# Kernel optimization log

Measured on AMD Instinct MI355X. Metric: run time of the kernel, lower is better.

Reference implementation:

```python
import jax, jax.numpy as jnp
import numpy as np

V_N = 50000   # nodes
E_N = 800000  # edges
DS, DV, R = 64, 8, 3
NB = 16       # rbf bases (scalar edge dim); vector edge dim = 1
DS_MSG = 2 * DS + NB      # 144
DV_MSG = 2 * DV + 1       # 17
EPS = 1e-8


def _gvp(s, Vv, Wh, Ws, bs, Wmu, Wg, bg, relu):
    # s: [E, ds_in], Vv: [E, R, dv_in]
    Vh = jnp.einsum('erd,dh->erh', Vv, Wh)                 # [E, R, h]
    vn = jnp.sqrt(jnp.sum(Vh * Vh, axis=-2) + EPS)         # [E, h]
    s_out = jnp.concatenate([s, vn], axis=-1) @ Ws + bs    # [E, ds_out]
    Vmu = jnp.einsum('erh,ho->ero', Vh, Wmu)               # [E, R, dv_out]
    gate = jax.nn.sigmoid(s_out @ Wg + bg)                 # vector gating
    V_out = Vmu * gate[:, None, :]
    if relu:
        s_out = jax.nn.relu(s_out)
    return s_out, V_out


def _make_gvp_params(key, ds_in, dv_in, ds_out, dv_out):
    h = max(dv_in, dv_out)
    ks = jax.random.split(key, 4)
    Wh = jax.random.normal(ks[0], (dv_in, h), jnp.float32) / np.sqrt(dv_in)
    Ws = jax.random.normal(ks[1], (ds_in + h, ds_out), jnp.float32) / np.sqrt(ds_in + h)
    bs = jnp.zeros((ds_out,), jnp.float32)
    Wmu = jax.random.normal(ks[2], (h, dv_out), jnp.float32) / np.sqrt(h)
    Wg = jax.random.normal(ks[3], (ds_out, dv_out), jnp.float32) / np.sqrt(ds_out)
    bg = jnp.zeros((dv_out,), jnp.float32)
    return Wh, Ws, bs, Wmu, Wg, bg


def setup_inputs() -> dict:
    key = jax.random.key(0)
    ks = jax.random.split(key, 8)
    inp = {
        's': jax.random.normal(ks[0], (V_N, DS), jnp.float32),
        'V': jax.random.normal(ks[1], (V_N, R, DV), jnp.float32),
        's_e': jax.random.normal(ks[2], (E_N, NB), jnp.float32),
        'V_e': jax.random.normal(ks[3], (E_N, R, 1), jnp.float32),
        'edge_index': jax.random.randint(ks[4], (2, E_N), 0, V_N, jnp.int64 if jax.config.jax_enable_x64 else jnp.int32),
    }
    p1 = _make_gvp_params(ks[5], DS_MSG, DV_MSG, DS, DV)
    p2 = _make_gvp_params(ks[6], DS, DV, DS, DV)
    p3 = _make_gvp_params(ks[7], DS, DV, DS, DV)
    for i, p in enumerate([p1, p2, p3], start=1):
        for name, w in zip(['Wh', 'Ws', 'bs', 'Wmu', 'Wg', 'bg'], p):
            inp[f'{name}{i}'] = w
    return inp


def reference(s, V, s_e, V_e, edge_index,
              Wh1, Ws1, bs1, Wmu1, Wg1, bg1,
              Wh2, Ws2, bs2, Wmu2, Wg2, bg2,
              Wh3, Ws3, bs3, Wmu3, Wg3, bg3):
    src, dest = edge_index[0], edge_index[1]
    s_cat = jnp.concatenate([s[src], s[dest], s_e], axis=-1)   # [E, DS_MSG]
    V_cat = jnp.concatenate([V[src], V[dest], V_e], axis=-1)   # [E, R, DV_MSG]
    s1, V1 = _gvp(s_cat, V_cat, Wh1, Ws1, bs1, Wmu1, Wg1, bg1, relu=True)
    s2, V2 = _gvp(s1, V1, Wh2, Ws2, bs2, Wmu2, Wg2, bg2, relu=True)
    s3, V3 = _gvp(s2, V2, Wh3, Ws3, bs3, Wmu3, Wg3, bg3, relu=False)
    return s3, V3
```

## Files before the change

### kernel.cpp

```cpp
#include <hip/hip_runtime.h>
#include <cstddef>

#define EN 800000
#define VN 50000

__global__ __launch_bounds__(256) void node_pre(
    const float* __restrict__ s, const float* __restrict__ V,
    const float* __restrict__ Wh1, const float* __restrict__ Ws1,
    float* __restrict__ A, float* __restrict__ B,
    float* __restrict__ VA, float* __restrict__ VB)
{
    const int tid  = threadIdx.x;
    const int lane = tid & 63;
    const int wv   = __builtin_amdgcn_readfirstlane(tid >> 6);

    float w[128];
    #pragma unroll
    for (int k = 0; k < 128; ++k) w[k] = Ws1[k * 64 + lane];

    const int hv = (lane < 51) ? (lane / 3) : 0;
    const int rv = (lane < 51) ? (lane % 3) : 0;
    float whA[8], whB[8];
    #pragma unroll
    for (int d = 0; d < 8; ++d) {
        whA[d] = Wh1[d * 17 + hv];
        whB[d] = Wh1[(8 + d) * 17 + hv];
    }

    const int nwaves = gridDim.x * 4;
    for (int v = blockIdx.x * 4 + wv; v < VN; v += nwaves) {
        const float* sv = s + (size_t)v * 64;
        float a = 0.f, b = 0.f;
        #pragma unroll
        for (int k = 0; k < 64; ++k) {
            float sk = sv[k];
            a += sk * w[k];
            b += sk * w[64 + k];
        }
        A[(size_t)v * 64 + lane] = a;
        B[(size_t)v * 64 + lane] = b;

        const float* vrow = V + (size_t)v * 24 + rv * 8;
        float va = 0.f, vb = 0.f;
        #pragma unroll
        for (int d = 0; d < 8; ++d) {
            float x = vrow[d];
            va += x * whA[d];
            vb += x * whB[d];
        }
        if (lane < 51) {
            VA[(size_t)v * 52 + lane] = va;
            VB[(size_t)v * 52 + lane] = vb;
        }
    }
}

__global__ __launch_bounds__(256, 2) void edge_kernel(
    const float* __restrict__ s_e, const float* __restrict__ V_e,
    const int* __restrict__ eidx,
    const float* __restrict__ Wh1, const float* __restrict__ Ws1, const float* __restrict__ bs1,
    const float* __restrict__ Wmu1, const float* __restrict__ Wg1, const float* __restrict__ bg1,
    const float* __restrict__ Wh2, const float* __restrict__ Ws2, const float* __restrict__ bs2,
    const float* __restrict__ Wmu2, const float* __restrict__ Wg2, const float* __restrict__ bg2,
    const float* __restrict__ Wh3, const float* __restrict__ Ws3, const float* __restrict__ bs3,
    const float* __restrict__ Wmu3, const float* __restrict__ Wg3, const float* __restrict__ bg3,
    const float* __restrict__ A, const float* __restrict__ B,
    const float* __restrict__ VA, const float* __restrict__ VB,
    float* __restrict__ out)
{
    __shared__ float buf[4][72][64];
    const int tid  = threadIdx.x;
    const int lane = tid & 63;
    const int wv   = tid >> 6;
    float (*wbuf)[64] = buf[wv];

    const int e   = blockIdx.x * 256 + tid;
    const int src = eidx[e];
    const int dst = eidx[EN + e];

    const float ve0 = V_e[(size_t)e * 3 + 0];
    const float ve1 = V_e[(size_t)e * 3 + 1];
    const float ve2 = V_e[(size_t)e * 3 + 2];

    float vmu[24];
    #pragma unroll
    for (int o = 0; o < 24; ++o) vmu[o] = 0.f;

    const float4* qa  = (const float4*)(VA + (size_t)src * 52);
    const float4* qb  = (const float4*)(VB + (size_t)dst * 52);
    const float*  w16 = Wh1 + 16 * 17;

    #pragma unroll 1
    for (int c = 0; c < 4; ++c) {
        float4 a0 = qa[3*c], a1 = qa[3*c+1], a2 = qa[3*c+2];
        float4 b0 = qb[3*c], b1 = qb[3*c+1], b2 = qb[3*c+2];
        float av[12] = {a0.x,a0.y,a0.z,a0.w, a1.x,a1.y,a1.z,a1.w, a2.x,a2.y,a2.z,a2.w};
        float bv[12] = {b0.x,b0.y,b0.z,b0.w, b1.x,b1.y,b1.z,b1.w, b2.x,b2.y,b2.z,b2.w};
        #pragma unroll
        for (int i = 0; i < 4; ++i) {
            const int h = 4*c + i;
            float ww = w16[h];
            float v0 = av[3*i+0] + bv[3*i+0] + ve0 * ww;
            float v1 = av[3*i+1] + bv[3*i+1] + ve1 * ww;
            float v2 = av[3*i+2] + bv[3*i+2] + ve2 * ww;
            wbuf[h][lane] = sqrtf(v0*v0 + v1*v1 + v2*v2 + 1e-8f);
            const float* wm = Wmu1 + h * 8;
            #pragma unroll
            for (int o = 0; o < 8; ++o) {
                float m = wm[o];
                vmu[o] += v0 * m; vmu[8+o] += v1 * m; vmu[16+o] += v2 * m;
            }
        }
    }
    {
        float4 a = qa[12], b = qb[12];
        float ww = w16[16];
        float v0 = a.x + b.x + ve0 * ww;
        float v1 = a.y + b.y + ve1 * ww;
        float v2 = a.z + b.z + ve2 * ww;
        wbuf[16][lane] = sqrtf(v0*v0 + v1*v1 + v2*v2 + 1e-8f);
        const float* wm = Wmu1 + 16 * 8;
        #pragma unroll
        for (int o = 0; o < 8; ++o) {
            float m = wm[o];
            vmu[o] += v0 * m; vmu[8+o] += v1 * m; vmu[16+o] += v2 * m;
        }
    }

    float acc[64];
    {
        const float4* fa = (const float4*)(A + (size_t)src * 64);
        const float4* fb = (const float4*)(B + (size_t)dst * 64);
        #pragma unroll
        for (int q = 0; q < 16; ++q) {
            float4 ta = fa[q], tb = fb[q];
            acc[4*q+0] = ta.x + tb.x + bs1[4*q+0];
            acc[4*q+1] = ta.y + tb.y + bs1[4*q+1];
            acc[4*q+2] = ta.z + tb.z + bs1[4*q+2];
            acc[4*q+3] = ta.w + tb.w + bs1[4*q+3];
        }
    }
    const float* pse = s_e + (size_t)e * 16;
    #pragma unroll 1
    for (int k = 0; k < 16; ++k) {
        float m = pse[k];
        const float* wr = Ws1 + (128 + k) * 64;
        #pragma unroll
        for (int j = 0; j < 64; ++j) acc[j] += m * wr[j];
    }
    #pragma unroll 1
    for (int k = 0; k < 17; ++k) {
        float m = wbuf[k][lane];
        const float* wr = Ws1 + (144 + k) * 64;
        #pragma unroll
        for (int j = 0; j < 64; ++j) acc[j] += m * wr[j];
    }

    float Vv[24];
    {
        float g[8];
        #pragma unroll
        for (int o = 0; o < 8; ++o) g[o] = bg1[o];
        #pragma unroll
        for (int j = 0; j < 64; ++j) {
            float sj = acc[j];
            const float* wg = Wg1 + j * 8;
            #pragma unroll
            for (int o = 0; o < 8; ++o) g[o] += sj * wg[o];
        }
        #pragma unroll
        for (int o = 0; o < 8; ++o) {
            float gg = 1.f / (1.f + __expf(-g[o]));
            Vv[o] = vmu[o] * gg; Vv[8+o] = vmu[8+o] * gg; Vv[16+o] = vmu[16+o] * gg;
        }
    }
    #pragma unroll
    for (int j = 0; j < 64; ++j) wbuf[j][lane] = fmaxf(acc[j], 0.f);

    #pragma unroll 1
    for (int t = 0; t < 2; ++t) {
        const float* Wh  = t ? Wh3  : Wh2;
        const float* Ws  = t ? Ws3  : Ws2;
        const float* bs  = t ? bs3  : bs2;
        const float* Wmu = t ? Wmu3 : Wmu2;
        const float* Wg  = t ? Wg3  : Wg2;
        const float* bg  = t ? bg3  : bg2;

        float vmu2[24];
        #pragma unroll
        for (int o = 0; o < 24; ++o) vmu2[o] = 0.f;
        #pragma unroll 1
        for (int h = 0; h < 8; ++h) {
            float v0 = 0.f, v1 = 0.f, v2 = 0.f;
            #pragma unroll
            for (int d = 0; d < 8; ++d) {
                float wd = Wh[d * 8 + h];
                v0 += Vv[d] * wd; v1 += Vv[8+d] * wd; v2 += Vv[16+d] * wd;
            }
            wbuf[64 + h][lane] = sqrtf(v0*v0 + v1*v1 + v2*v2 + 1e-8f);
            const float* wm = Wmu + h * 8;
            #pragma unroll
            for (int o = 0; o < 8; ++o) {
                float m = wm[o];
                vmu2[o] += v0 * m; vmu2[8+o] += v1 * m; vmu2[16+o] += v2 * m;
            }
        }

        #pragma unroll
        for (int j = 0; j < 64; ++j) acc[j] = bs[j];
        #pragma unroll 1
        for (int k = 0; k < 72; ++k) {
            float m = wbuf[k][lane];
            const float* wr = Ws + k * 64;
            #pragma unroll
            for (int j = 0; j < 64; ++j) acc[j] += m * wr[j];
        }

        float g[8];
        #pragma unroll
        for (int o = 0; o < 8; ++o) g[o] = bg[o];
        #pragma unroll
        for (int j = 0; j < 64; ++j) {
            float sj = acc[j];
            const float* wg = Wg + j * 8;
            #pragma unroll
            for (int o = 0; o < 8; ++o) g[o] += sj * wg[o];
        }
        #pragma unroll
        for (int o = 0; o < 8; ++o) {
            float gg = 1.f / (1.f + __expf(-g[o]));
            Vv[o] = vmu2[o] * gg; Vv[8+o] = vmu2[8+o] * gg; Vv[16+o] = vmu2[16+o] * gg;
        }
        if (t == 0) {
            #pragma unroll
            for (int j = 0; j < 64; ++j) wbuf[j][lane] = fmaxf(acc[j], 0.f);
        }
    }

    float4* po = (float4*)(out + (size_t)e * 64);
    #pragma unroll
    for (int q = 0; q < 16; ++q) {
        float4 tq; tq.x = acc[4*q]; tq.y = acc[4*q+1]; tq.z = acc[4*q+2]; tq.w = acc[4*q+3];
        po[q] = tq;
    }
    float4* pv = (float4*)(out + (size_t)EN * 64 + (size_t)e * 24);
    #pragma unroll
    for (int q = 0; q < 6; ++q) {
        float4 tq; tq.x = Vv[4*q]; tq.y = Vv[4*q+1]; tq.z = Vv[4*q+2]; tq.w = Vv[4*q+3];
        pv[q] = tq;
    }
}

extern "C" void kernel_launch(void* const* d_in, const int* in_sizes, int n_in,
                              void* d_out, int out_size, void* d_ws, size_t ws_size,
                              hipStream_t stream)
{
    const float* s    = (const float*)d_in[0];
    const float* V    = (const float*)d_in[1];
    const float* s_e  = (const float*)d_in[2];
    const float* V_e  = (const float*)d_in[3];
    const int*   eidx = (const int*)d_in[4];
    const float* Wh1 = (const float*)d_in[5];
    const float* Ws1 = (const float*)d_in[6];
    const float* bs1 = (const float*)d_in[7];
    const float* Wmu1= (const float*)d_in[8];
    const float* Wg1 = (const float*)d_in[9];
    const float* bg1 = (const float*)d_in[10];
    const float* Wh2 = (const float*)d_in[11];
    const float* Ws2 = (const float*)d_in[12];
    const float* bs2 = (const float*)d_in[13];
    const float* Wmu2= (const float*)d_in[14];
    const float* Wg2 = (const float*)d_in[15];
    const float* bg2 = (const float*)d_in[16];
    const float* Wh3 = (const float*)d_in[17];
    const float* Ws3 = (const float*)d_in[18];
    const float* bs3 = (const float*)d_in[19];
    const float* Wmu3= (const float*)d_in[20];
    const float* Wg3 = (const float*)d_in[21];
    const float* bg3 = (const float*)d_in[22];

    float* ws  = (float*)d_ws;
    float* A   = ws;
    float* B   = A + 3200000;
    float* VA  = B + 3200000;
    float* VB  = VA + 2600000;
    float* out = (float*)d_out;

    hipLaunchKernelGGL(node_pre, dim3(512), dim3(256), 0, stream,
                       s, V, Wh1, Ws1, A, B, VA, VB);
    hipLaunchKernelGGL(edge_kernel, dim3(EN / 256), dim3(256), 0, stream,
                       s_e, V_e, eidx,
                       Wh1, Ws1, bs1, Wmu1, Wg1, bg1,
                       Wh2, Ws2, bs2, Wmu2, Wg2, bg2,
                       Wh3, Ws3, bs3, Wmu3, Wg3, bg3,
                       A, B, VA, VB, out);
}
```

Measured before the change: 1.309 ms.

## Drop LDS staging; use output buffer as scratch and vector weight loads via VGPR

Removes the per-wave shared-memory buffer. Vector norms are kept in registers, and the intermediate relu'd scalar features are written to the global output row and re-read for the next layer. Weight reads go through float4 loads with a fake VGPR zero offset, which makes them vector-memory loads instead of scalar loads. The occupancy hint is raised to 3 blocks. The aim is to lift the LDS occupancy limit and cut load instruction count, at the cost of extra global traffic and possible register pressure.

```diff
diff --git a/kernel.cpp b/kernel.cpp
--- a/kernel.cpp
+++ b/kernel.cpp
@@ -3,6 +3,13 @@
 
 #define EN 800000
 #define VN 50000
+
+__device__ __forceinline__ float4 ld4(const float* p, int z) {
+    return *(const float4*)(p + z);
+}
+__device__ __forceinline__ float ld1(const float* p, int z) {
+    return p[z];
+}
 
 __global__ __launch_bounds__(256) void node_pre(
     const float* __restrict__ s, const float* __restrict__ V,
@@ -55,7 +62,7 @@
     }
 }
 
-__global__ __launch_bounds__(256, 2) void edge_kernel(
+__global__ __launch_bounds__(256, 3) void edge_kernel(
     const float* __restrict__ s_e, const float* __restrict__ V_e,
     const int* __restrict__ eidx,
     const float* __restrict__ Wh1, const float* __restrict__ Ws1, const float* __restrict__ bs1,
@@ -68,12 +75,10 @@
     const float* __restrict__ VA, const float* __restrict__ VB,
     float* __restrict__ out)
 {
-    __shared__ float buf[4][72][64];
-    const int tid  = threadIdx.x;
-    const int lane = tid & 63;
-    const int wv   = tid >> 6;
-    float (*wbuf)[64] = buf[wv];
-
+    int z;
+    asm volatile("v_mov_b32 %0, 0" : "=v"(z));
+
+    const int tid = threadIdx.x;
     const int e   = blockIdx.x * 256 + tid;
     const int src = eidx[e];
     const int dst = eidx[EN + e];
@@ -82,15 +87,26 @@
     const float ve1 = V_e[(size_t)e * 3 + 1];
     const float ve2 = V_e[(size_t)e * 3 + 2];
 
+    float wv16[17];
+    {
+        const float* p = Wh1 + 16 * 17;
+        #pragma unroll
+        for (int q = 0; q < 4; ++q) {
+            float4 t = ld4(p + 4 * q, z);
+            wv16[4*q] = t.x; wv16[4*q+1] = t.y; wv16[4*q+2] = t.z; wv16[4*q+3] = t.w;
+        }
+        wv16[16] = ld1(p + 16, z);
+    }
+
+    float vn[17];
     float vmu[24];
     #pragma unroll
     for (int o = 0; o < 24; ++o) vmu[o] = 0.f;
 
-    const float4* qa  = (const float4*)(VA + (size_t)src * 52);
-    const float4* qb  = (const float4*)(VB + (size_t)dst * 52);
-    const float*  w16 = Wh1 + 16 * 17;
-
-    #pragma unroll 1
+    const float4* qa = (const float4*)(VA + (size_t)src * 52);
+    const float4* qb = (const float4*)(VB + (size_t)dst * 52);
+
+    #pragma unroll
     for (int c = 0; c < 4; ++c) {
         float4 a0 = qa[3*c], a1 = qa[3*c+1], a2 = qa[3*c+2];
         float4 b0 = qb[3*c], b1 = qb[3*c+1], b2 = qb[3*c+2];
@@ -99,32 +115,36 @@
         #pragma unroll
         for (int i = 0; i < 4; ++i) {
             const int h = 4*c + i;
-            float ww = w16[h];
+            float ww = wv16[h];
             float v0 = av[3*i+0] + bv[3*i+0] + ve0 * ww;
             float v1 = av[3*i+1] + bv[3*i+1] + ve1 * ww;
             float v2 = av[3*i+2] + bv[3*i+2] + ve2 * ww;
-            wbuf[h][lane] = sqrtf(v0*v0 + v1*v1 + v2*v2 + 1e-8f);
-            const float* wm = Wmu1 + h * 8;
-            #pragma unroll
-            for (int o = 0; o < 8; ++o) {
-                float m = wm[o];
-                vmu[o] += v0 * m; vmu[8+o] += v1 * m; vmu[16+o] += v2 * m;
-            }
+            vn[h] = sqrtf(v0*v0 + v1*v1 + v2*v2 + 1e-8f);
+            float4 m0 = ld4(Wmu1 + h * 8, z);
+            float4 m1 = ld4(Wmu1 + h * 8 + 4, z);
+            vmu[0]  += v0*m0.x; vmu[1]  += v0*m0.y; vmu[2]  += v0*m0.z; vmu[3]  += v0*m0.w;
+            vmu[4]  += v0*m1.x; vmu[5]  += v0*m1.y; vmu[6]  += v0*m1.z; vmu[7]  += v0*m1.w;
+            vmu[8]  += v1*m0.x; vmu[9]  += v1*m0.y; vmu[10] += v1*m0.z; vmu[11] += v1*m0.w;
+            vmu[12] += v1*m1.x; vmu[13] += v1*m1.y; vmu[14] += v1*m1.z; vmu[15] += v1*m1.w;
+            vmu[16] += v2*m0.x; vmu[17] += v2*m0.y; vmu[18] += v2*m0.z; vmu[19] += v2*m0.w;
+            vmu[20] += v2*m1.x; vmu[21] += v2*m1.y; vmu[22] += v2*m1.z; vmu[23] += v2*m1.w;
         }
     }
     {
         float4 a = qa[12], b = qb[12];
-        float ww = w16[16];
+        float ww = wv16[16];
         float v0 = a.x + b.x + ve0 * ww;
         float v1 = a.y + b.y + ve1 * ww;
         float v2 = a.z + b.z + ve2 * ww;
-        wbuf[16][lane] = sqrtf(v0*v0 + v1*v1 + v2*v2 + 1e-8f);
-        const float* wm = Wmu1 + 16 * 8;
-        #pragma unroll
-        for (int o = 0; o < 8; ++o) {
-            float m = wm[o];
-            vmu[o] += v0 * m; vmu[8+o] += v1 * m; vmu[16+o] += v2 * m;
-        }
+        vn[16] = sqrtf(v0*v0 + v1*v1 + v2*v2 + 1e-8f);
+        float4 m0 = ld4(Wmu1 + 16 * 8, z);
+        float4 m1 = ld4(Wmu1 + 16 * 8 + 4, z);
+        vmu[0]  += v0*m0.x; vmu[1]  += v0*m0.y; vmu[2]  += v0*m0.z; vmu[3]  += v0*m0.w;
+        vmu[4]  += v0*m1.x; vmu[5]  += v0*m1.y; vmu[6]  += v0*m1.z; vmu[7]  += v0*m1.w;
+        vmu[8]  += v1*m0.x; vmu[9]  += v1*m0.y; vmu[10] += v1*m0.z; vmu[11] += v1*m0.w;
+        vmu[12] += v1*m1.x; vmu[13] += v1*m1.y; vmu[14] += v1*m1.z; vmu[15] += v1*m1.w;
+        vmu[16] += v2*m0.x; vmu[17] += v2*m0.y; vmu[18] += v2*m0.z; vmu[19] += v2*m0.w;
+        vmu[20] += v2*m1.x; vmu[21] += v2*m1.y; vmu[22] += v2*m1.z; vmu[23] += v2*m1.w;
     }
 
     float acc[64];
@@ -134,48 +154,69 @@
         #pragma unroll
         for (int q = 0; q < 16; ++q) {
             float4 ta = fa[q], tb = fb[q];
-            acc[4*q+0] = ta.x + tb.x + bs1[4*q+0];
-            acc[4*q+1] = ta.y + tb.y + bs1[4*q+1];
-            acc[4*q+2] = ta.z + tb.z + bs1[4*q+2];
-            acc[4*q+3] = ta.w + tb.w + bs1[4*q+3];
-        }
-    }
-    const float* pse = s_e + (size_t)e * 16;
-    #pragma unroll 1
-    for (int k = 0; k < 16; ++k) {
-        float m = pse[k];
-        const float* wr = Ws1 + (128 + k) * 64;
-        #pragma unroll
-        for (int j = 0; j < 64; ++j) acc[j] += m * wr[j];
-    }
-    #pragma unroll 1
+            float4 bb = ld4(bs1 + 4 * q, z);
+            acc[4*q+0] = ta.x + tb.x + bb.x;
+            acc[4*q+1] = ta.y + tb.y + bb.y;
+            acc[4*q+2] = ta.z + tb.z + bb.z;
+            acc[4*q+3] = ta.w + tb.w + bb.w;
+        }
+    }
+    {
+        const float4* ps = (const float4*)(s_e + (size_t)e * 16);
+        float4 e0 = ps[0], e1 = ps[1], e2 = ps[2], e3 = ps[3];
+        float mm[16] = {e0.x,e0.y,e0.z,e0.w, e1.x,e1.y,e1.z,e1.w,
+                        e2.x,e2.y,e2.z,e2.w, e3.x,e3.y,e3.z,e3.w};
+        #pragma unroll
+        for (int k = 0; k < 16; ++k) {
+            const float* wr = Ws1 + (128 + k) * 64;
+            float m = mm[k];
+            #pragma unroll
+            for (int q = 0; q < 16; ++q) {
+                float4 w = ld4(wr + 4 * q, z);
+                acc[4*q+0] += m * w.x; acc[4*q+1] += m * w.y;
+                acc[4*q+2] += m * w.z; acc[4*q+3] += m * w.w;
+            }
+        }
+    }
+    #pragma unroll
     for (int k = 0; k < 17; ++k) {
-        float m = wbuf[k][lane];
         const float* wr = Ws1 + (144 + k) * 64;
-        #pragma unroll
-        for (int j = 0; j < 64; ++j) acc[j] += m * wr[j];
+        float m = vn[k];
+        #pragma unroll
+        for (int q = 0; q < 16; ++q) {
+            float4 w = ld4(wr + 4 * q, z);
+            acc[4*q+0] += m * w.x; acc[4*q+1] += m * w.y;
+            acc[4*q+2] += m * w.z; acc[4*q+3] += m * w.w;
+        }
     }
 
     float Vv[24];
     {
         float g[8];
-        #pragma unroll
-        for (int o = 0; o < 8; ++o) g[o] = bg1[o];
+        float4 b0 = ld4(bg1, z), b1 = ld4(bg1 + 4, z);
+        g[0]=b0.x; g[1]=b0.y; g[2]=b0.z; g[3]=b0.w;
+        g[4]=b1.x; g[5]=b1.y; g[6]=b1.z; g[7]=b1.w;
         #pragma unroll
         for (int j = 0; j < 64; ++j) {
             float sj = acc[j];
-            const float* wg = Wg1 + j * 8;
-            #pragma unroll
-            for (int o = 0; o < 8; ++o) g[o] += sj * wg[o];
+            float4 wa = ld4(Wg1 + j * 8, z), wb = ld4(Wg1 + j * 8 + 4, z);
+            g[0] += sj*wa.x; g[1] += sj*wa.y; g[2] += sj*wa.z; g[3] += sj*wa.w;
+            g[4] += sj*wb.x; g[5] += sj*wb.y; g[6] += sj*wb.z; g[7] += sj*wb.w;
         }
         #pragma unroll
         for (int o = 0; o < 8; ++o) {
             float gg = 1.f / (1.f + __expf(-g[o]));
-            Vv[o] = vmu[o] * gg; Vv[8+o] = vmu[8+o] * gg; Vv[16+o] = vmu[16+o] * gg;
-        }
-    }
-    #pragma unroll
-    for (int j = 0; j < 64; ++j) wbuf[j][lane] = fmaxf(acc[j], 0.f);
+            Vv[o] = vmu[o]*gg; Vv[8+o] = vmu[8+o]*gg; Vv[16+o] = vmu[16+o]*gg;
+        }
+    }
+    float* soS = out + (size_t)e * 64;
+    #pragma unroll
+    for (int q = 0; q < 16; ++q) {
+        float4 t;
+        t.x = fmaxf(acc[4*q+0], 0.f); t.y = fmaxf(acc[4*q+1], 0.f);
+        t.z = fmaxf(acc[4*q+2], 0.f); t.w = fmaxf(acc[4*q+3], 0.f);
+        ((float4*)soS)[q] = t;
+    }
 
     #pragma unroll 1
     for (int t = 0; t < 2; ++t) {
@@ -186,63 +227,107 @@
         const float* Wg  = t ? Wg3  : Wg2;
         const float* bg  = t ? bg3  : bg2;
 
+        float whv[64], wmv[64];
+        #pragma unroll
+        for (int q = 0; q < 16; ++q) {
+            float4 a = ld4(Wh + 4 * q, z);
+            whv[4*q]=a.x; whv[4*q+1]=a.y; whv[4*q+2]=a.z; whv[4*q+3]=a.w;
+            float4 b = ld4(Wmu + 4 * q, z);
+            wmv[4*q]=b.x; wmv[4*q+1]=b.y; wmv[4*q+2]=b.z; wmv[4*q+3]=b.w;
+        }
+        float vn2[8];
         float vmu2[24];
         #pragma unroll
         for (int o = 0; o < 24; ++o) vmu2[o] = 0.f;
-        #pragma unroll 1
+        #pragma unroll
         for (int h = 0; h < 8; ++h) {
             float v0 = 0.f, v1 = 0.f, v2 = 0.f;
             #pragma unroll
             for (int d = 0; d < 8; ++d) {
-                float wd = Wh[d * 8 + h];
-                v0 += Vv[d] * wd; v1 += Vv[8+d] * wd; v2 += Vv[16+d] * wd;
-            }
-            wbuf[64 + h][lane] = sqrtf(v0*v0 + v1*v1 + v2*v2 + 1e-8f);
-            const float* wm = Wmu + h * 8;
+                float wd = whv[d * 8 + h];
+                v0 += Vv[d]*wd; v1 += Vv[8+d]*wd; v2 += Vv[16+d]*wd;
+            }
+            vn2[h] = sqrtf(v0*v0 + v1*v1 + v2*v2 + 1e-8f);
             #pragma unroll
             for (int o = 0; o < 8; ++o) {
-                float m = wm[o];
-                vmu2[o] += v0 * m; vmu2[8+o] += v1 * m; vmu2[16+o] += v2 * m;
-            }
-        }
-
-        #pragma unroll
-        for (int j = 0; j < 64; ++j) acc[j] = bs[j];
+                float m = wmv[h * 8 + o];
+                vmu2[o] += v0*m; vmu2[8+o] += v1*m; vmu2[16+o] += v2*m;
+            }
+        }
+
+        float acc2[64];
+        #pragma unroll
+        for (int q = 0; q < 16; ++q) {
+            float4 bb = ld4(bs + 4 * q, z);
+            acc2[4*q]=bb.x; acc2[4*q+1]=bb.y; acc2[4*q+2]=bb.z; acc2[4*q+3]=bb.w;
+        }
         #pragma unroll 1
-        for (int k = 0; k < 72; ++k) {
-            float m = wbuf[k][lane];
-            const float* wr = Ws + k * 64;
-            #pragma unroll
-            for (int j = 0; j < 64; ++j) acc[j] += m * wr[j];
+        for (int c = 0; c < 16; ++c) {
+            float4 mv = *(const float4*)(soS + 4 * c);
+            const float* wr = Ws + (4 * c) * 64;
+            float m4[4] = {mv.x, mv.y, mv.z, mv.w};
+            #pragma unroll
+            for (int i = 0; i < 4; ++i) {
+                float m = m4[i];
+                const float* wri = wr + i * 64;
+                #pragma unroll
+                for (int q = 0; q < 16; ++q) {
+                    float4 w = ld4(wri + 4 * q, z);
+                    acc2[4*q+0] += m * w.x; acc2[4*q+1] += m * w.y;
+                    acc2[4*q+2] += m * w.z; acc2[4*q+3] += m * w.w;
+                }
+            }
+        }
+        #pragma unroll
+        for (int k = 0; k < 8; ++k) {
+            const float* wr = Ws + (64 + k) * 64;
+            float m = vn2[k];
+            #pragma unroll
+            for (int q = 0; q < 16; ++q) {
+                float4 w = ld4(wr + 4 * q, z);
+                acc2[4*q+0] += m * w.x; acc2[4*q+1] += m * w.y;
+                acc2[4*q+2] += m * w.z; acc2[4*q+3] += m * w.w;
+            }
         }
 
         float g[8];
-        #pragma unroll
-        for (int o = 0; o < 8; ++o) g[o] = bg[o];
+        {
+            float4 b0 = ld4(bg, z), b1 = ld4(bg + 4, z);
+            g[0]=b0.x; g[1]=b0.y; g[2]=b0.z; g[3]=b0.w;
+            g[4]=b1.x; g[5]=b1.y; g[6]=b1.z; g[7]=b1.w;
+        }
         #pragma unroll
         for (int j = 0; j < 64; ++j) {
-            float sj = acc[j];
-            const float* wg = Wg + j * 8;
-            #pragma unroll
-            for (int o = 0; o < 8; ++o) g[o] += sj * wg[o];
+            float sj = acc2[j];
+            float4 wa = ld4(Wg + j * 8, z), wb = ld4(Wg + j * 8 + 4, z);
+            g[0] += sj*wa.x; g[1] += sj*wa.y; g[2] += sj*wa.z; g[3] += sj*wa.w;
+            g[4] += sj*wb.x; g[5] += sj*wb.y; g[6] += sj*wb.z; g[7] += sj*wb.w;
         }
         #pragma unroll
         for (int o = 0; o < 8; ++o) {
             float gg = 1.f / (1.f + __expf(-g[o]));
-            Vv[o] = vmu2[o] * gg; Vv[8+o] = vmu2[8+o] * gg; Vv[16+o] = vmu2[16+o] * gg;
-        }
+            Vv[o] = vmu2[o]*gg; Vv[8+o] = vmu2[8+o]*gg; Vv[16+o] = vmu2[16+o]*gg;
+        }
+
         if (t == 0) {
             #pragma unroll
-            for (int j = 0; j < 64; ++j) wbuf[j][lane] = fmaxf(acc[j], 0.f);
-        }
-    }
-
-    float4* po = (float4*)(out + (size_t)e * 64);
-    #pragma unroll
-    for (int q = 0; q < 16; ++q) {
-        float4 tq; tq.x = acc[4*q]; tq.y = acc[4*q+1]; tq.z = acc[4*q+2]; tq.w = acc[4*q+3];
-        po[q] = tq;
-    }
+            for (int q = 0; q < 16; ++q) {
+                float4 tq;
+                tq.x = fmaxf(acc2[4*q+0], 0.f); tq.y = fmaxf(acc2[4*q+1], 0.f);
+                tq.z = fmaxf(acc2[4*q+2], 0.f); tq.w = fmaxf(acc2[4*q+3], 0.f);
+                ((float4*)soS)[q] = tq;
+            }
+        } else {
+            #pragma unroll
+            for (int q = 0; q < 16; ++q) {
+                float4 tq;
+                tq.x = acc2[4*q+0]; tq.y = acc2[4*q+1];
+                tq.z = acc2[4*q+2]; tq.w = acc2[4*q+3];
+                ((float4*)soS)[q] = tq;
+            }
+        }
+    }
+
     float4* pv = (float4*)(out + (size_t)EN * 64 + (size_t)e * 24);
     #pragma unroll
     for (int q = 0; q < 6; ++q) {
```

Result: slower. 3.371 ms (+157.4%).
